# Performance work log

Hardware: AMD Instinct MI355X
Metric: run time of the kernel (lower is better)

The kernel has to match this reference:

```python
import jax, jax.numpy as jnp
import numpy as np

N_HEADS = 8
EMBED_DIM = 512
HEAD_DIM = EMBED_DIM // N_HEADS
INPUT_DIM = 512


def setup_inputs() -> dict:
    key = jax.random.key(0)
    ks = jax.random.split(key, 9)
    B, N = 4, 2048
    s_in = 1.0 / np.sqrt(INPUT_DIM)
    s_e = 1.0 / np.sqrt(EMBED_DIM)
    return {
        "q": jax.random.normal(ks[0], (B, N, INPUT_DIM), dtype=jnp.float32),
        "wq": jax.random.uniform(ks[1], (EMBED_DIM, INPUT_DIM), jnp.float32, -s_in, s_in),
        "bq": jax.random.uniform(ks[2], (EMBED_DIM,), jnp.float32, -s_in, s_in),
        "wk": jax.random.uniform(ks[3], (EMBED_DIM, INPUT_DIM), jnp.float32, -s_in, s_in),
        "bk": jax.random.uniform(ks[4], (EMBED_DIM,), jnp.float32, -s_in, s_in),
        "wv": jax.random.uniform(ks[5], (EMBED_DIM, INPUT_DIM), jnp.float32, -s_in, s_in),
        "bv": jax.random.uniform(ks[6], (EMBED_DIM,), jnp.float32, -s_in, s_in),
        "wo": jax.random.uniform(ks[7], (EMBED_DIM, EMBED_DIM), jnp.float32, -s_e, s_e),
        "bo": jax.random.uniform(ks[8], (EMBED_DIM,), jnp.float32, -s_e, s_e),
    }


def reference(q, wq, bq, wk, bk, wv, bv, wo, bo):
    B, N, _ = q.shape
    # linear projections (torch Linear: x @ W.T + b)
    Q = (q @ wq.T + bq).reshape(B, N, N_HEADS, HEAD_DIM).transpose(0, 2, 1, 3)
    K = (q @ wk.T + bk).reshape(B, N, N_HEADS, HEAD_DIM).transpose(0, 2, 1, 3)
    V = (q @ wv.T + bv).reshape(B, N, N_HEADS, HEAD_DIM).transpose(0, 2, 1, 3)
    scores = jnp.einsum("bhqd,bhkd->bhqk", Q, K) / jnp.sqrt(
        jnp.asarray(HEAD_DIM, dtype=q.dtype)
    )
    weights = jax.nn.softmax(scores, axis=-1)
    out = jnp.einsum("bhqk,bhkd->bhqd", weights, V)  # [B,H,N,Dh]
    out = out.transpose(0, 2, 1, 3).reshape(B, N, EMBED_DIM)
    return out @ wo.T + bo
```

## Files before the change

### kernel.cpp

```cpp
#include <hip/hip_runtime.h>
#include <hip/hip_bf16.h>
#include <math.h>

#define SEQ    2048
#define DH     64
#define EMB    512
#define INDIM  512
#define NHEADS 8
#define BATCH  4
#define MTOT   (BATCH * SEQ)

typedef __attribute__((ext_vector_type(8))) short bf16x8;
typedef __attribute__((ext_vector_type(4))) float f32x4;

__device__ __forceinline__ ushort f2bf(float x) {
  union { float f; unsigned u; } v; v.f = x;
  unsigned r = v.u + 0x7FFFu + ((v.u >> 16) & 1u);
  return (ushort)(r >> 16);
}

__device__ __forceinline__ unsigned cvt_pk_bf16(float lo, float hi) {
  unsigned r;
  asm("v_cvt_pk_bf16_f32 %0, %1, %2" : "=v"(r) : "v"(lo), "v"(hi));
  return r;
}

__device__ __forceinline__ float fast_exp2(float x) {
  float r;
  asm("v_exp_f32 %0, %1" : "=v"(r) : "v"(x));
  return r;
}

__device__ __forceinline__ void permswap32(unsigned &x, unsigned &y) {
  asm("v_permlane32_swap_b32 %0, %1" : "+v"(x), "+v"(y));
}

__global__ __launch_bounds__(256) void conv_bf16(const float* __restrict__ src,
                                                 ushort* __restrict__ dst, int n8) {
  const int i = blockIdx.x * 256 + threadIdx.x;
  if (i >= n8) return;
  const float4 a = ((const float4*)src)[i * 2];
  const float4 b = ((const float4*)src)[i * 2 + 1];
  uint4 o;
  o.x = cvt_pk_bf16(a.x, a.y);
  o.y = cvt_pk_bf16(a.z, a.w);
  o.z = cvt_pk_bf16(b.x, b.y);
  o.w = cvt_pk_bf16(b.z, b.w);
  ((uint4*)dst)[i] = o;
}

__global__ __launch_bounds__(256) void conv_bf16_w4(
    const float* __restrict__ w0, const float* __restrict__ w1,
    const float* __restrict__ w2, const float* __restrict__ w3,
    ushort* __restrict__ dst, int n8per) {
  const int i = blockIdx.x * 256 + threadIdx.x;
  if (i >= n8per) return;
  const float* src = (blockIdx.y == 0) ? w0 : (blockIdx.y == 1) ? w1
                   : (blockIdx.y == 2) ? w2 : w3;
  ushort* d = dst + (size_t)blockIdx.y * n8per * 8;
  const float4 a = ((const float4*)src)[i * 2];
  const float4 b = ((const float4*)src)[i * 2 + 1];
  uint4 o;
  o.x = cvt_pk_bf16(a.x, a.y);
  o.y = cvt_pk_bf16(a.z, a.w);
  o.z = cvt_pk_bf16(b.x, b.y);
  o.w = cvt_pk_bf16(b.z, b.w);
  ((uint4*)d)[i] = o;
}

template <int MODE>
__global__ __launch_bounds__(256) void mfma_gemm(
    const ushort* __restrict__ A, const ushort* __restrict__ W,
    const float* __restrict__ b0, const float* __restrict__ b1,
    const float* __restrict__ b2,
    ushort* __restrict__ outQ, ushort* __restrict__ outK,
    ushort* __restrict__ outVT, float* __restrict__ outF) {
  __shared__ __align__(16) char smem[MODE == 0 ? 35840 : 16384];
  ushort* As = (ushort*)smem;
  ushort* Bs = (ushort*)(smem + 8192);
  ushort* Tl = (ushort*)smem;
  ushort* Tl2 = (ushort*)smem;

  const int bm = blockIdx.x * 128;
  const int bn = blockIdx.y * 128;
  const int tid = threadIdx.x;
  const int wave = tid >> 6, lane = tid & 63;
  const int g = lane >> 4, ln = lane & 15;
  const int wr = wave >> 1, wc = wave & 1;

  f32x4 acc[4][4];
#pragma unroll
  for (int m = 0; m < 4; ++m)
#pragma unroll
    for (int n = 0; n < 4; ++n) acc[m][n] = (f32x4){0.f, 0.f, 0.f, 0.f};

  const size_t a_base = (size_t)(bm + wave * 16 + (lane >> 2)) * INDIM + (lane & 3) * 8;
  const size_t b_base = (size_t)(bn + wave * 16 + (lane >> 2)) * INDIM + (lane & 3) * 8;
  ushort* ldsA0 = As + wave * 512;
  ushort* ldsA1 = As + 2048 + wave * 512;
  ushort* ldsB0 = Bs + wave * 512;
  ushort* ldsB1 = Bs + 2048 + wave * 512;

  for (int k0 = 0; k0 < INDIM; k0 += 32) {
    __syncthreads();
    __builtin_amdgcn_global_load_lds(
        (const __attribute__((address_space(1))) void*)(A + a_base + k0),
        (__attribute__((address_space(3))) void*)ldsA0, 16, 0, 0);
    __builtin_amdgcn_global_load_lds(
        (const __attribute__((address_space(1))) void*)(A + a_base + 64 * INDIM + k0),
        (__attribute__((address_space(3))) void*)ldsA1, 16, 0, 0);
    __builtin_amdgcn_global_load_lds(
        (const __attribute__((address_space(1))) void*)(W + b_base + k0),
        (__attribute__((address_space(3))) void*)ldsB0, 16, 0, 0);
    __builtin_amdgcn_global_load_lds(
        (const __attribute__((address_space(1))) void*)(W + b_base + 64 * INDIM + k0),
        (__attribute__((address_space(3))) void*)ldsB1, 16, 0, 0);
    __syncthreads();

    bf16x8 af[4], bfv[4];
#pragma unroll
    for (int m = 0; m < 4; ++m)
      af[m] = *(const bf16x8*)&As[(64 * wr + 16 * m + ln) * 32 + 8 * g];
#pragma unroll
    for (int n = 0; n < 4; ++n)
      bfv[n] = *(const bf16x8*)&Bs[(64 * wc + 16 * n + ln) * 32 + 8 * g];
#pragma unroll
    for (int m = 0; m < 4; ++m)
#pragma unroll
      for (int n = 0; n < 4; ++n)
        acc[m][n] = __builtin_amdgcn_mfma_f32_16x16x32_bf16(af[m], bfv[n], acc[m][n], 0, 0, 0);
  }

  if (MODE == 1) {
#pragma unroll
    for (int n = 0; n < 4; ++n) {
      const int e = bn + 64 * wc + 16 * n + ln;
      const float bv = b0[e];
#pragma unroll
      for (int m = 0; m < 4; ++m)
#pragma unroll
        for (int r = 0; r < 4; ++r) {
          const int row = bm + 64 * wr + 16 * m + 4 * g + r;
          outF[(size_t)row * EMB + e] = acc[m][n][r] + bv;
        }
    }
    return;
  }

  const int which = bn >> 9;
  const float* bias = (which == 0) ? b0 : (which == 1) ? b1 : b2;

  if (which < 2) {
    const float scl = (which == 0) ? 0.18033688f : 1.0f;
    ushort* dst = (which == 0) ? outQ : outK;
    __syncthreads();
#pragma unroll
    for (int n = 0; n < 4; ++n) {
      const int cl = 64 * wc + 16 * n + ln;
      const float bv = bias[(bn & 511) + cl];
#pragma unroll
      for (int m = 0; m < 4; ++m)
#pragma unroll
        for (int r = 0; r < 4; ++r) {
          const int rl = 64 * wr + 16 * m + 4 * g + r;
          Tl2[rl * 136 + cl] = f2bf((acc[m][n][r] + bv) * scl);
        }
    }
    __syncthreads();
#pragma unroll
    for (int j = 0; j < 8; ++j) {
      const int cid = j * 256 + tid;
      const int seg = cid >> 3;
      const int l8 = cid & 7;
      const int rl = seg >> 1, half = seg & 1;
      const int row = bm + rl;
      const int b = row >> 11, nn = row & (SEQ - 1);
      const int h = ((bn & 511) >> 6) + half;
      const bf16x8 v = *(const bf16x8*)&Tl2[rl * 136 + half * 64 + l8 * 8];
      *(bf16x8*)&dst[(((size_t)(b * NHEADS + h) * SEQ) + nn) * DH + l8 * 8] = v;
    }
  } else {
    __syncthreads();
#pragma unroll
    for (int n = 0; n < 4; ++n) {
      const int cl = 64 * wc + 16 * n + ln;
      const float bv = bias[(bn & 511) + cl];
#pragma unroll
      for (int m = 0; m < 4; ++m)
#pragma unroll
        for (int r = 0; r < 4; ++r) {
          const int rl = 64 * wr + 16 * m + 4 * g + r;
          Tl[cl * 140 + rl] = f2bf(acc[m][n][r] + bv);
        }
    }
    __syncthreads();
    const int c = tid >> 1;
    const int rh = (tid & 1) * 64;
    const int e = (bn & 511) + c;
    const int h = e >> 6, d = e & 63;
    const int b = bm >> 11;
    const int nn0 = (bm & (SEQ - 1)) + rh;
    ushort* drow = outVT + (((size_t)(b * NHEADS + h) * DH) + d) * SEQ + nn0;
#pragma unroll
    for (int j = 0; j < 8; ++j)
      *(bf16x8*)&drow[j * 8] = *(const bf16x8*)&Tl[c * 140 + rh + j * 8];
  }
}

__global__ __launch_bounds__(256) void attn_mfma(const ushort* __restrict__ Q,
                                                 const ushort* __restrict__ K,
                                                 const ushort* __restrict__ VT,
                                                 ushort* __restrict__ O) {
  __shared__ __align__(16) ushort Kl[2][64 * 72];
  __shared__ __align__(16) ushort Vl[2][64 * 72];

  const int tid = threadIdx.x;
  const int wave = tid >> 6, lane = tid & 63;
  const int g = lane >> 4, ln = lane & 15;

  const int orig = blockIdx.x;
  const int swz = (orig & 7) * 64 + (orig >> 3);
  const int bh = swz >> 4;
  const int qx = swz & 15;
  const int qbase = qx * 128 + wave * 32;

  const ushort* Qb = Q + ((size_t)bh * SEQ + qbase) * DH;
  const ushort* Kb = K + (size_t)bh * SEQ * DH;
  const ushort* Vb = VT + (size_t)bh * DH * SEQ;

  const bf16x8 qfA0 = *(const bf16x8*)&Qb[ln * DH + 8 * g];
  const bf16x8 qfA1 = *(const bf16x8*)&Qb[ln * DH + 32 + 8 * g];
  const bf16x8 qfB0 = *(const bf16x8*)&Qb[(16 + ln) * DH + 8 * g];
  const bf16x8 qfB1 = *(const bf16x8*)&Qb[(16 + ln) * DH + 32 + 8 * g];

  bf16x8 vones;
#pragma unroll
  for (int i = 0; i < 8; ++i) vones[i] = (short)0x3F80;

  f32x4 oaccA[4], oaccB[4];
  f32x4 oaccDA = (f32x4){0.f, 0.f, 0.f, 0.f};
  f32x4 oaccDB = (f32x4){0.f, 0.f, 0.f, 0.f};
#pragma unroll
  for (int t = 0; t < 4; ++t) {
    oaccA[t] = (f32x4){0.f, 0.f, 0.f, 0.f};
    oaccB[t] = (f32x4){0.f, 0.f, 0.f, 0.f};
  }

  const int skv = tid >> 3, sd = (tid & 7) * 8;
  const int dt = tid >> 2, kc = (tid & 3) * 8;
  const int pr0 = skv ^ (((((skv >> 2) ^ (skv >> 3)) & 1)) * 12);
  const int s32 = skv + 32;
  const int pr1 = s32 ^ (((((s32 >> 2) ^ (s32 >> 3)) & 1)) * 12);

  bf16x8 k0v = *(const bf16x8*)&Kb[(size_t)skv * DH + sd];
  bf16x8 k1v = *(const bf16x8*)&Kb[(size_t)(32 + skv) * DH + sd];
  bf16x8 v0v = *(const bf16x8*)&Vb[(size_t)dt * SEQ + kc];
  bf16x8 v1v = *(const bf16x8*)&Vb[(size_t)dt * SEQ + 32 + kc];
  *(bf16x8*)&Kl[0][pr0 * 72 + sd] = k0v;
  *(bf16x8*)&Kl[0][pr1 * 72 + sd] = k1v;
  *(bf16x8*)&Vl[0][dt * 72 + kc] = v0v;
  *(bf16x8*)&Vl[0][dt * 72 + 32 + kc] = v1v;
  k0v = *(const bf16x8*)&Kb[(size_t)(64 + skv) * DH + sd];
  k1v = *(const bf16x8*)&Kb[(size_t)(96 + skv) * DH + sd];
  v0v = *(const bf16x8*)&Vb[(size_t)dt * SEQ + 64 + kc];
  v1v = *(const bf16x8*)&Vb[(size_t)dt * SEQ + 96 + kc];
  asm volatile("s_waitcnt lgkmcnt(0)" ::: "memory");
  __builtin_amdgcn_s_barrier();

  for (int it = 0; it < 32; ++it) {
    const int cur = it & 1;
    ushort* Kc = Kl[cur];
    ushort* Vc = Vl[cur];

    if (it < 31) {
      ushort* Kn = Kl[cur ^ 1];
      ushort* Vn = Vl[cur ^ 1];
      *(bf16x8*)&Kn[pr0 * 72 + sd] = k0v;
      *(bf16x8*)&Kn[pr1 * 72 + sd] = k1v;
      *(bf16x8*)&Vn[dt * 72 + kc] = v0v;
      *(bf16x8*)&Vn[dt * 72 + 32 + kc] = v1v;
    }
    {
      const int nxt = (it + 2 < 32) ? (it + 2) * 64 : 31 * 64;
      k0v = *(const bf16x8*)&Kb[(size_t)(nxt + skv) * DH + sd];
      k1v = *(const bf16x8*)&Kb[(size_t)(nxt + 32 + skv) * DH + sd];
      v0v = *(const bf16x8*)&Vb[(size_t)dt * SEQ + nxt + kc];
      v1v = *(const bf16x8*)&Vb[(size_t)dt * SEQ + nxt + 32 + kc];
    }

    bf16x8 ka[4][2], vb[2][4];
#pragma unroll
    for (int t = 0; t < 4; ++t) {
      ka[t][0] = *(const bf16x8*)&Kc[(16 * t + ln) * 72 + 8 * g];
      ka[t][1] = *(const bf16x8*)&Kc[(16 * t + ln) * 72 + 32 + 8 * g];
    }
#pragma unroll
    for (int c = 0; c < 2; ++c)
#pragma unroll
      for (int t = 0; t < 4; ++t)
        vb[c][t] = *(const bf16x8*)&Vc[(16 * t + ln) * 72 + 32 * c + 8 * g];

    f32x4 sA0 = (f32x4){0.f, 0.f, 0.f, 0.f};
    f32x4 sA1 = sA0, sA2 = sA0, sA3 = sA0;
    f32x4 sB0 = sA0, sB1 = sA0, sB2 = sA0, sB3 = sA0;
    __builtin_amdgcn_s_setprio(1);
    sA0 = __builtin_amdgcn_mfma_f32_16x16x32_bf16(ka[0][0], qfA0, sA0, 0, 0, 0);
    sB0 = __builtin_amdgcn_mfma_f32_16x16x32_bf16(ka[0][0], qfB0, sB0, 0, 0, 0);
    sA1 = __builtin_amdgcn_mfma_f32_16x16x32_bf16(ka[1][0], qfA0, sA1, 0, 0, 0);
    sB1 = __builtin_amdgcn_mfma_f32_16x16x32_bf16(ka[1][0], qfB0, sB1, 0, 0, 0);
    sA2 = __builtin_amdgcn_mfma_f32_16x16x32_bf16(ka[2][0], qfA0, sA2, 0, 0, 0);
    sB2 = __builtin_amdgcn_mfma_f32_16x16x32_bf16(ka[2][0], qfB0, sB2, 0, 0, 0);
    sA3 = __builtin_amdgcn_mfma_f32_16x16x32_bf16(ka[3][0], qfA0, sA3, 0, 0, 0);
    sB3 = __builtin_amdgcn_mfma_f32_16x16x32_bf16(ka[3][0], qfB0, sB3, 0, 0, 0);
    sA0 = __builtin_amdgcn_mfma_f32_16x16x32_bf16(ka[0][1], qfA1, sA0, 0, 0, 0);
    sB0 = __builtin_amdgcn_mfma_f32_16x16x32_bf16(ka[0][1], qfB1, sB0, 0, 0, 0);
    sA1 = __builtin_amdgcn_mfma_f32_16x16x32_bf16(ka[1][1], qfA1, sA1, 0, 0, 0);
    sB1 = __builtin_amdgcn_mfma_f32_16x16x32_bf16(ka[1][1], qfB1, sB1, 0, 0, 0);
    sA2 = __builtin_amdgcn_mfma_f32_16x16x32_bf16(ka[2][1], qfA1, sA2, 0, 0, 0);
    sB2 = __builtin_amdgcn_mfma_f32_16x16x32_bf16(ka[2][1], qfB1, sB2, 0, 0, 0);
    sA3 = __builtin_amdgcn_mfma_f32_16x16x32_bf16(ka[3][1], qfA1, sA3, 0, 0, 0);
    sB3 = __builtin_amdgcn_mfma_f32_16x16x32_bf16(ka[3][1], qfB1, sB3, 0, 0, 0);
    __builtin_amdgcn_s_setprio(0);

    float pA0[4], pA1[4], pA2[4], pA3[4];
    float pB0[4], pB1[4], pB2[4], pB3[4];
#pragma unroll
    for (int r = 0; r < 4; ++r) {
      pA0[r] = fast_exp2(sA0[r]);
      pA1[r] = fast_exp2(sA1[r]);
      pA2[r] = fast_exp2(sA2[r]);
      pA3[r] = fast_exp2(sA3[r]);
      pB0[r] = fast_exp2(sB0[r]);
      pB1[r] = fast_exp2(sB1[r]);
      pB2[r] = fast_exp2(sB2[r]);
      pB3[r] = fast_exp2(sB3[r]);
    }

    unsigned aa0 = cvt_pk_bf16(pA0[0], pA0[1]);
    unsigned aa2 = cvt_pk_bf16(pA1[0], pA1[1]);
    unsigned aa1 = cvt_pk_bf16(pA0[2], pA0[3]);
    unsigned aa3 = cvt_pk_bf16(pA1[2], pA1[3]);
    permswap32(aa0, aa2);
    permswap32(aa1, aa3);
    unsigned ab0 = cvt_pk_bf16(pA2[0], pA2[1]);
    unsigned ab2 = cvt_pk_bf16(pA3[0], pA3[1]);
    unsigned ab1 = cvt_pk_bf16(pA2[2], pA2[3]);
    unsigned ab3 = cvt_pk_bf16(pA3[2], pA3[3]);
    permswap32(ab0, ab2);
    permswap32(ab1, ab3);
    unsigned ba0 = cvt_pk_bf16(pB0[0], pB0[1]);
    unsigned ba2 = cvt_pk_bf16(pB1[0], pB1[1]);
    unsigned ba1 = cvt_pk_bf16(pB0[2], pB0[3]);
    unsigned ba3 = cvt_pk_bf16(pB1[2], pB1[3]);
    permswap32(ba0, ba2);
    permswap32(ba1, ba3);
    unsigned bb0 = cvt_pk_bf16(pB2[0], pB2[1]);
    unsigned bb2 = cvt_pk_bf16(pB3[0], pB3[1]);
    unsigned bb1 = cvt_pk_bf16(pB2[2], pB2[3]);
    unsigned bb3 = cvt_pk_bf16(pB3[2], pB3[3]);
    permswap32(bb0, bb2);
    permswap32(bb1, bb3);
    union { unsigned u[4]; bf16x8 v; } paA0, paA1, paB0, paB1;
    paA0.u[0] = aa0; paA0.u[1] = aa1; paA0.u[2] = aa2; paA0.u[3] = aa3;
    paA1.u[0] = ab0; paA1.u[1] = ab1; paA1.u[2] = ab2; paA1.u[3] = ab3;
    paB0.u[0] = ba0; paB0.u[1] = ba1; paB0.u[2] = ba2; paB0.u[3] = ba3;
    paB1.u[0] = bb0; paB1.u[1] = bb1; paB1.u[2] = bb2; paB1.u[3] = bb3;

    __builtin_amdgcn_s_setprio(1);
#pragma unroll
    for (int t = 0; t < 4; ++t) {
      oaccA[t] = __builtin_amdgcn_mfma_f32_16x16x32_bf16(paA0.v, vb[0][t], oaccA[t], 0, 0, 0);
      oaccB[t] = __builtin_amdgcn_mfma_f32_16x16x32_bf16(paB0.v, vb[0][t], oaccB[t], 0, 0, 0);
      oaccA[t] = __builtin_amdgcn_mfma_f32_16x16x32_bf16(paA1.v, vb[1][t], oaccA[t], 0, 0, 0);
      oaccB[t] = __builtin_amdgcn_mfma_f32_16x16x32_bf16(paB1.v, vb[1][t], oaccB[t], 0, 0, 0);
    }
    oaccDA = __builtin_amdgcn_mfma_f32_16x16x32_bf16(paA0.v, vones, oaccDA, 0, 0, 0);
    oaccDB = __builtin_amdgcn_mfma_f32_16x16x32_bf16(paB0.v, vones, oaccDB, 0, 0, 0);
    oaccDA = __builtin_amdgcn_mfma_f32_16x16x32_bf16(paA1.v, vones, oaccDA, 0, 0, 0);
    oaccDB = __builtin_amdgcn_mfma_f32_16x16x32_bf16(paB1.v, vones, oaccDB, 0, 0, 0);
    __builtin_amdgcn_s_setprio(0);

    asm volatile("s_waitcnt lgkmcnt(0)" ::: "memory");
    __builtin_amdgcn_s_barrier();
  }

  const int b = bh >> 3, h = bh & 7;
#pragma unroll
  for (int r = 0; r < 4; ++r) {
    const float irA = 1.0f / oaccDA[r];
    const float irB = 1.0f / oaccDB[r];
    ushort* opA = O + ((size_t)(b * SEQ) + qbase + 4 * g + r) * EMB + h * 64;
    ushort* opB = O + ((size_t)(b * SEQ) + qbase + 16 + 4 * g + r) * EMB + h * 64;
#pragma unroll
    for (int t = 0; t < 4; ++t) {
      opA[16 * t + ln] = f2bf(oaccA[t][r] * irA);
      opB[16 * t + ln] = f2bf(oaccB[t][r] * irB);
    }
  }
}

extern "C" void kernel_launch(void* const* d_in, const int* in_sizes, int n_in,
                              void* d_out, int out_size, void* d_ws, size_t ws_size,
                              hipStream_t stream) {
  const float* q  = (const float*)d_in[0];
  const float* wq = (const float*)d_in[1];
  const float* bq = (const float*)d_in[2];
  const float* wk = (const float*)d_in[3];
  const float* bk = (const float*)d_in[4];
  const float* wv = (const float*)d_in[5];
  const float* bv = (const float*)d_in[6];
  const float* wo = (const float*)d_in[7];
  const float* bo = (const float*)d_in[8];
  float* out = (float*)d_out;

  const size_t XSZ = (size_t)MTOT * INDIM;
  const size_t WSZ = (size_t)EMB * INDIM;
  const size_t QSZ = (size_t)BATCH * NHEADS * SEQ * DH;
  ushort* wsX = (ushort*)d_ws;
  ushort* wsW = wsX + XSZ;
  ushort* wsQ = wsW + 4 * WSZ;
  ushort* wsK = wsQ + QSZ;
  ushort* wsVT = wsK + QSZ;
  ushort* wsA = wsVT + QSZ;

  const dim3 blk(256);

  conv_bf16<<<dim3(XSZ / 8 / 256), blk, 0, stream>>>(q, wsX, XSZ / 8);
  conv_bf16_w4<<<dim3(WSZ / 8 / 256, 4), blk, 0, stream>>>(wq, wk, wv, wo, wsW, WSZ / 8);

  mfma_gemm<0><<<dim3(MTOT / 128, 1536 / 128), blk, 0, stream>>>(
      wsX, wsW, bq, bk, bv, wsQ, wsK, wsVT, nullptr);

  attn_mfma<<<dim3(512), blk, 0, stream>>>(wsQ, wsK, wsVT, wsA);

  mfma_gemm<1><<<dim3(MTOT / 128, EMB / 128), blk, 0, stream>>>(
      wsA, wsW + 3 * WSZ, bo, nullptr, nullptr, nullptr, nullptr, nullptr, out);
}
```

Baseline: 100.9 us.

## Double attention KV tile to 128 and halve output-projection M tile

The attention kernel now stages 128 KV rows per iteration instead of 64, running two 64-row sub-steps per barrier. This halves the number of loop iterations and block-wide barriers and issues larger prefetches. The output-projection GEMM uses a 64-row M tile, doubling its grid from 256 to 512 blocks to fill more CUs. In exchange, attention LDS use and register pressure rise, which may lower occupancy, and the smaller GEMM tile has less data reuse per block.

```diff
diff --git a/kernel.cpp b/kernel.cpp
--- a/kernel.cpp
+++ b/kernel.cpp
@@ -75,22 +75,24 @@
     const float* __restrict__ b2,
     ushort* __restrict__ outQ, ushort* __restrict__ outK,
     ushort* __restrict__ outVT, float* __restrict__ outF) {
-  __shared__ __align__(16) char smem[MODE == 0 ? 35840 : 16384];
+  constexpr int BM = (MODE == 0) ? 128 : 64;
+  constexpr int MF = (MODE == 0) ? 4 : 2;
+  __shared__ __align__(16) char smem[MODE == 0 ? 35840 : 12288];
   ushort* As = (ushort*)smem;
-  ushort* Bs = (ushort*)(smem + 8192);
+  ushort* Bs = (ushort*)(smem + (MODE == 0 ? 8192 : 4096));
   ushort* Tl = (ushort*)smem;
   ushort* Tl2 = (ushort*)smem;
 
-  const int bm = blockIdx.x * 128;
+  const int bm = blockIdx.x * BM;
   const int bn = blockIdx.y * 128;
   const int tid = threadIdx.x;
   const int wave = tid >> 6, lane = tid & 63;
   const int g = lane >> 4, ln = lane & 15;
   const int wr = wave >> 1, wc = wave & 1;
 
-  f32x4 acc[4][4];
-#pragma unroll
-  for (int m = 0; m < 4; ++m)
+  f32x4 acc[MF][4];
+#pragma unroll
+  for (int m = 0; m < MF; ++m)
 #pragma unroll
     for (int n = 0; n < 4; ++n) acc[m][n] = (f32x4){0.f, 0.f, 0.f, 0.f};
 
@@ -106,9 +108,10 @@
     __builtin_amdgcn_global_load_lds(
         (const __attribute__((address_space(1))) void*)(A + a_base + k0),
         (__attribute__((address_space(3))) void*)ldsA0, 16, 0, 0);
-    __builtin_amdgcn_global_load_lds(
-        (const __attribute__((address_space(1))) void*)(A + a_base + 64 * INDIM + k0),
-        (__attribute__((address_space(3))) void*)ldsA1, 16, 0, 0);
+    if (MODE == 0)
+      __builtin_amdgcn_global_load_lds(
+          (const __attribute__((address_space(1))) void*)(A + a_base + 64 * INDIM + k0),
+          (__attribute__((address_space(3))) void*)ldsA1, 16, 0, 0);
     __builtin_amdgcn_global_load_lds(
         (const __attribute__((address_space(1))) void*)(W + b_base + k0),
         (__attribute__((address_space(3))) void*)ldsB0, 16, 0, 0);
@@ -117,15 +120,15 @@
         (__attribute__((address_space(3))) void*)ldsB1, 16, 0, 0);
     __syncthreads();
 
-    bf16x8 af[4], bfv[4];
-#pragma unroll
-    for (int m = 0; m < 4; ++m)
-      af[m] = *(const bf16x8*)&As[(64 * wr + 16 * m + ln) * 32 + 8 * g];
+    bf16x8 af[MF], bfv[4];
+#pragma unroll
+    for (int m = 0; m < MF; ++m)
+      af[m] = *(const bf16x8*)&As[((MODE == 0 ? 64 : 32) * wr + 16 * m + ln) * 32 + 8 * g];
 #pragma unroll
     for (int n = 0; n < 4; ++n)
       bfv[n] = *(const bf16x8*)&Bs[(64 * wc + 16 * n + ln) * 32 + 8 * g];
 #pragma unroll
-    for (int m = 0; m < 4; ++m)
+    for (int m = 0; m < MF; ++m)
 #pragma unroll
       for (int n = 0; n < 4; ++n)
         acc[m][n] = __builtin_amdgcn_mfma_f32_16x16x32_bf16(af[m], bfv[n], acc[m][n], 0, 0, 0);
@@ -137,10 +140,10 @@
       const int e = bn + 64 * wc + 16 * n + ln;
       const float bv = b0[e];
 #pragma unroll
-      for (int m = 0; m < 4; ++m)
+      for (int m = 0; m < MF; ++m)
 #pragma unroll
         for (int r = 0; r < 4; ++r) {
-          const int row = bm + 64 * wr + 16 * m + 4 * g + r;
+          const int row = bm + 32 * wr + 16 * m + 4 * g + r;
           outF[(size_t)row * EMB + e] = acc[m][n][r] + bv;
         }
     }
@@ -211,8 +214,8 @@
                                                  const ushort* __restrict__ K,
                                                  const ushort* __restrict__ VT,
                                                  ushort* __restrict__ O) {
-  __shared__ __align__(16) ushort Kl[2][64 * 72];
-  __shared__ __align__(16) ushort Vl[2][64 * 72];
+  __shared__ __align__(16) ushort Kl[2][128 * 72];
+  __shared__ __align__(16) ushort Vl[2][64 * 136];
 
   const int tid = threadIdx.x;
   const int wave = tid >> 6, lane = tid & 63;
@@ -248,137 +251,149 @@
 
   const int skv = tid >> 3, sd = (tid & 7) * 8;
   const int dt = tid >> 2, kc = (tid & 3) * 8;
-  const int pr0 = skv ^ (((((skv >> 2) ^ (skv >> 3)) & 1)) * 12);
-  const int s32 = skv + 32;
-  const int pr1 = s32 ^ (((((s32 >> 2) ^ (s32 >> 3)) & 1)) * 12);
-
-  bf16x8 k0v = *(const bf16x8*)&Kb[(size_t)skv * DH + sd];
-  bf16x8 k1v = *(const bf16x8*)&Kb[(size_t)(32 + skv) * DH + sd];
-  bf16x8 v0v = *(const bf16x8*)&Vb[(size_t)dt * SEQ + kc];
-  bf16x8 v1v = *(const bf16x8*)&Vb[(size_t)dt * SEQ + 32 + kc];
-  *(bf16x8*)&Kl[0][pr0 * 72 + sd] = k0v;
-  *(bf16x8*)&Kl[0][pr1 * 72 + sd] = k1v;
-  *(bf16x8*)&Vl[0][dt * 72 + kc] = v0v;
-  *(bf16x8*)&Vl[0][dt * 72 + 32 + kc] = v1v;
-  k0v = *(const bf16x8*)&Kb[(size_t)(64 + skv) * DH + sd];
-  k1v = *(const bf16x8*)&Kb[(size_t)(96 + skv) * DH + sd];
-  v0v = *(const bf16x8*)&Vb[(size_t)dt * SEQ + 64 + kc];
-  v1v = *(const bf16x8*)&Vb[(size_t)dt * SEQ + 96 + kc];
+  int pr[4];
+#pragma unroll
+  for (int j = 0; j < 4; ++j) {
+    const int row = skv + 32 * j;
+    pr[j] = row ^ (((((row >> 2) ^ (row >> 3)) & 1)) * 12);
+  }
+
+  bf16x8 kv[4], vv[4];
+#pragma unroll
+  for (int j = 0; j < 4; ++j) {
+    kv[j] = *(const bf16x8*)&Kb[(size_t)(skv + 32 * j) * DH + sd];
+    vv[j] = *(const bf16x8*)&Vb[(size_t)dt * SEQ + kc + 32 * j];
+  }
+#pragma unroll
+  for (int j = 0; j < 4; ++j) {
+    *(bf16x8*)&Kl[0][pr[j] * 72 + sd] = kv[j];
+    *(bf16x8*)&Vl[0][dt * 136 + kc + 32 * j] = vv[j];
+  }
+#pragma unroll
+  for (int j = 0; j < 4; ++j) {
+    kv[j] = *(const bf16x8*)&Kb[(size_t)(128 + skv + 32 * j) * DH + sd];
+    vv[j] = *(const bf16x8*)&Vb[(size_t)dt * SEQ + 128 + kc + 32 * j];
+  }
   asm volatile("s_waitcnt lgkmcnt(0)" ::: "memory");
   __builtin_amdgcn_s_barrier();
 
-  for (int it = 0; it < 32; ++it) {
+  for (int it = 0; it < 16; ++it) {
     const int cur = it & 1;
-    ushort* Kc = Kl[cur];
-    ushort* Vc = Vl[cur];
-
-    if (it < 31) {
+    const ushort* Kc = Kl[cur];
+    const ushort* Vc = Vl[cur];
+
+    if (it < 15) {
       ushort* Kn = Kl[cur ^ 1];
       ushort* Vn = Vl[cur ^ 1];
-      *(bf16x8*)&Kn[pr0 * 72 + sd] = k0v;
-      *(bf16x8*)&Kn[pr1 * 72 + sd] = k1v;
-      *(bf16x8*)&Vn[dt * 72 + kc] = v0v;
-      *(bf16x8*)&Vn[dt * 72 + 32 + kc] = v1v;
+#pragma unroll
+      for (int j = 0; j < 4; ++j) {
+        *(bf16x8*)&Kn[pr[j] * 72 + sd] = kv[j];
+        *(bf16x8*)&Vn[dt * 136 + kc + 32 * j] = vv[j];
+      }
     }
     {
-      const int nxt = (it + 2 < 32) ? (it + 2) * 64 : 31 * 64;
-      k0v = *(const bf16x8*)&Kb[(size_t)(nxt + skv) * DH + sd];
-      k1v = *(const bf16x8*)&Kb[(size_t)(nxt + 32 + skv) * DH + sd];
-      v0v = *(const bf16x8*)&Vb[(size_t)dt * SEQ + nxt + kc];
-      v1v = *(const bf16x8*)&Vb[(size_t)dt * SEQ + nxt + 32 + kc];
-    }
-
-    bf16x8 ka[4][2], vb[2][4];
-#pragma unroll
-    for (int t = 0; t < 4; ++t) {
-      ka[t][0] = *(const bf16x8*)&Kc[(16 * t + ln) * 72 + 8 * g];
-      ka[t][1] = *(const bf16x8*)&Kc[(16 * t + ln) * 72 + 32 + 8 * g];
-    }
-#pragma unroll
-    for (int c = 0; c < 2; ++c)
-#pragma unroll
-      for (int t = 0; t < 4; ++t)
-        vb[c][t] = *(const bf16x8*)&Vc[(16 * t + ln) * 72 + 32 * c + 8 * g];
-
-    f32x4 sA0 = (f32x4){0.f, 0.f, 0.f, 0.f};
-    f32x4 sA1 = sA0, sA2 = sA0, sA3 = sA0;
-    f32x4 sB0 = sA0, sB1 = sA0, sB2 = sA0, sB3 = sA0;
-    __builtin_amdgcn_s_setprio(1);
-    sA0 = __builtin_amdgcn_mfma_f32_16x16x32_bf16(ka[0][0], qfA0, sA0, 0, 0, 0);
-    sB0 = __builtin_amdgcn_mfma_f32_16x16x32_bf16(ka[0][0], qfB0, sB0, 0, 0, 0);
-    sA1 = __builtin_amdgcn_mfma_f32_16x16x32_bf16(ka[1][0], qfA0, sA1, 0, 0, 0);
-    sB1 = __builtin_amdgcn_mfma_f32_16x16x32_bf16(ka[1][0], qfB0, sB1, 0, 0, 0);
-    sA2 = __builtin_amdgcn_mfma_f32_16x16x32_bf16(ka[2][0], qfA0, sA2, 0, 0, 0);
-    sB2 = __builtin_amdgcn_mfma_f32_16x16x32_bf16(ka[2][0], qfB0, sB2, 0, 0, 0);
-    sA3 = __builtin_amdgcn_mfma_f32_16x16x32_bf16(ka[3][0], qfA0, sA3, 0, 0, 0);
-    sB3 = __builtin_amdgcn_mfma_f32_16x16x32_bf16(ka[3][0], qfB0, sB3, 0, 0, 0);
-    sA0 = __builtin_amdgcn_mfma_f32_16x16x32_bf16(ka[0][1], qfA1, sA0, 0, 0, 0);
-    sB0 = __builtin_amdgcn_mfma_f32_16x16x32_bf16(ka[0][1], qfB1, sB0, 0, 0, 0);
-    sA1 = __builtin_amdgcn_mfma_f32_16x16x32_bf16(ka[1][1], qfA1, sA1, 0, 0, 0);
-    sB1 = __builtin_amdgcn_mfma_f32_16x16x32_bf16(ka[1][1], qfB1, sB1, 0, 0, 0);
-    sA2 = __builtin_amdgcn_mfma_f32_16x16x32_bf16(ka[2][1], qfA1, sA2, 0, 0, 0);
-    sB2 = __builtin_amdgcn_mfma_f32_16x16x32_bf16(ka[2][1], qfB1, sB2, 0, 0, 0);
-    sA3 = __builtin_amdgcn_mfma_f32_16x16x32_bf16(ka[3][1], qfA1, sA3, 0, 0, 0);
-    sB3 = __builtin_amdgcn_mfma_f32_16x16x32_bf16(ka[3][1], qfB1, sB3, 0, 0, 0);
-    __builtin_amdgcn_s_setprio(0);
-
-    float pA0[4], pA1[4], pA2[4], pA3[4];
-    float pB0[4], pB1[4], pB2[4], pB3[4];
-#pragma unroll
-    for (int r = 0; r < 4; ++r) {
-      pA0[r] = fast_exp2(sA0[r]);
-      pA1[r] = fast_exp2(sA1[r]);
-      pA2[r] = fast_exp2(sA2[r]);
-      pA3[r] = fast_exp2(sA3[r]);
-      pB0[r] = fast_exp2(sB0[r]);
-      pB1[r] = fast_exp2(sB1[r]);
-      pB2[r] = fast_exp2(sB2[r]);
-      pB3[r] = fast_exp2(sB3[r]);
-    }
-
-    unsigned aa0 = cvt_pk_bf16(pA0[0], pA0[1]);
-    unsigned aa2 = cvt_pk_bf16(pA1[0], pA1[1]);
-    unsigned aa1 = cvt_pk_bf16(pA0[2], pA0[3]);
-    unsigned aa3 = cvt_pk_bf16(pA1[2], pA1[3]);
-    permswap32(aa0, aa2);
-    permswap32(aa1, aa3);
-    unsigned ab0 = cvt_pk_bf16(pA2[0], pA2[1]);
-    unsigned ab2 = cvt_pk_bf16(pA3[0], pA3[1]);
-    unsigned ab1 = cvt_pk_bf16(pA2[2], pA2[3]);
-    unsigned ab3 = cvt_pk_bf16(pA3[2], pA3[3]);
-    permswap32(ab0, ab2);
-    permswap32(ab1, ab3);
-    unsigned ba0 = cvt_pk_bf16(pB0[0], pB0[1]);
-    unsigned ba2 = cvt_pk_bf16(pB1[0], pB1[1]);
-    unsigned ba1 = cvt_pk_bf16(pB0[2], pB0[3]);
-    unsigned ba3 = cvt_pk_bf16(pB1[2], pB1[3]);
-    permswap32(ba0, ba2);
-    permswap32(ba1, ba3);
-    unsigned bb0 = cvt_pk_bf16(pB2[0], pB2[1]);
-    unsigned bb2 = cvt_pk_bf16(pB3[0], pB3[1]);
-    unsigned bb1 = cvt_pk_bf16(pB2[2], pB2[3]);
-    unsigned bb3 = cvt_pk_bf16(pB3[2], pB3[3]);
-    permswap32(bb0, bb2);
-    permswap32(bb1, bb3);
-    union { unsigned u[4]; bf16x8 v; } paA0, paA1, paB0, paB1;
-    paA0.u[0] = aa0; paA0.u[1] = aa1; paA0.u[2] = aa2; paA0.u[3] = aa3;
-    paA1.u[0] = ab0; paA1.u[1] = ab1; paA1.u[2] = ab2; paA1.u[3] = ab3;
-    paB0.u[0] = ba0; paB0.u[1] = ba1; paB0.u[2] = ba2; paB0.u[3] = ba3;
-    paB1.u[0] = bb0; paB1.u[1] = bb1; paB1.u[2] = bb2; paB1.u[3] = bb3;
-
-    __builtin_amdgcn_s_setprio(1);
-#pragma unroll
-    for (int t = 0; t < 4; ++t) {
-      oaccA[t] = __builtin_amdgcn_mfma_f32_16x16x32_bf16(paA0.v, vb[0][t], oaccA[t], 0, 0, 0);
-      oaccB[t] = __builtin_amdgcn_mfma_f32_16x16x32_bf16(paB0.v, vb[0][t], oaccB[t], 0, 0, 0);
-      oaccA[t] = __builtin_amdgcn_mfma_f32_16x16x32_bf16(paA1.v, vb[1][t], oaccA[t], 0, 0, 0);
-      oaccB[t] = __builtin_amdgcn_mfma_f32_16x16x32_bf16(paB1.v, vb[1][t], oaccB[t], 0, 0, 0);
-    }
-    oaccDA = __builtin_amdgcn_mfma_f32_16x16x32_bf16(paA0.v, vones, oaccDA, 0, 0, 0);
-    oaccDB = __builtin_amdgcn_mfma_f32_16x16x32_bf16(paB0.v, vones, oaccDB, 0, 0, 0);
-    oaccDA = __builtin_amdgcn_mfma_f32_16x16x32_bf16(paA1.v, vones, oaccDA, 0, 0, 0);
-    oaccDB = __builtin_amdgcn_mfma_f32_16x16x32_bf16(paB1.v, vones, oaccDB, 0, 0, 0);
-    __builtin_amdgcn_s_setprio(0);
+      const int nxt = (it + 2 < 16) ? (it + 2) * 128 : 15 * 128;
+#pragma unroll
+      for (int j = 0; j < 4; ++j) {
+        kv[j] = *(const bf16x8*)&Kb[(size_t)(nxt + skv + 32 * j) * DH + sd];
+        vv[j] = *(const bf16x8*)&Vb[(size_t)dt * SEQ + nxt + kc + 32 * j];
+      }
+    }
+
+#pragma unroll
+    for (int s = 0; s < 2; ++s) {
+      bf16x8 ka[4][2], vb[2][4];
+#pragma unroll
+      for (int t = 0; t < 4; ++t) {
+        ka[t][0] = *(const bf16x8*)&Kc[(64 * s + 16 * t + ln) * 72 + 8 * g];
+        ka[t][1] = *(const bf16x8*)&Kc[(64 * s + 16 * t + ln) * 72 + 32 + 8 * g];
+      }
+#pragma unroll
+      for (int c = 0; c < 2; ++c)
+#pragma unroll
+        for (int t = 0; t < 4; ++t)
+          vb[c][t] = *(const bf16x8*)&Vc[(16 * t + ln) * 136 + 64 * s + 32 * c + 8 * g];
+
+      f32x4 sA0 = (f32x4){0.f, 0.f, 0.f, 0.f};
+      f32x4 sA1 = sA0, sA2 = sA0, sA3 = sA0;
+      f32x4 sB0 = sA0, sB1 = sA0, sB2 = sA0, sB3 = sA0;
+      __builtin_amdgcn_s_setprio(1);
+      sA0 = __builtin_amdgcn_mfma_f32_16x16x32_bf16(ka[0][0], qfA0, sA0, 0, 0, 0);
+      sB0 = __builtin_amdgcn_mfma_f32_16x16x32_bf16(ka[0][0], qfB0, sB0, 0, 0, 0);
+      sA1 = __builtin_amdgcn_mfma_f32_16x16x32_bf16(ka[1][0], qfA0, sA1, 0, 0, 0);
+      sB1 = __builtin_amdgcn_mfma_f32_16x16x32_bf16(ka[1][0], qfB0, sB1, 0, 0, 0);
+      sA2 = __builtin_amdgcn_mfma_f32_16x16x32_bf16(ka[2][0], qfA0, sA2, 0, 0, 0);
+      sB2 = __builtin_amdgcn_mfma_f32_16x16x32_bf16(ka[2][0], qfB0, sB2, 0, 0, 0);
+      sA3 = __builtin_amdgcn_mfma_f32_16x16x32_bf16(ka[3][0], qfA0, sA3, 0, 0, 0);
+      sB3 = __builtin_amdgcn_mfma_f32_16x16x32_bf16(ka[3][0], qfB0, sB3, 0, 0, 0);
+      sA0 = __builtin_amdgcn_mfma_f32_16x16x32_bf16(ka[0][1], qfA1, sA0, 0, 0, 0);
+      sB0 = __builtin_amdgcn_mfma_f32_16x16x32_bf16(ka[0][1], qfB1, sB0, 0, 0, 0);
+      sA1 = __builtin_amdgcn_mfma_f32_16x16x32_bf16(ka[1][1], qfA1, sA1, 0, 0, 0);
+      sB1 = __builtin_amdgcn_mfma_f32_16x16x32_bf16(ka[1][1], qfB1, sB1, 0, 0, 0);
+      sA2 = __builtin_amdgcn_mfma_f32_16x16x32_bf16(ka[2][1], qfA1, sA2, 0, 0, 0);
+      sB2 = __builtin_amdgcn_mfma_f32_16x16x32_bf16(ka[2][1], qfB1, sB2, 0, 0, 0);
+      sA3 = __builtin_amdgcn_mfma_f32_16x16x32_bf16(ka[3][1], qfA1, sA3, 0, 0, 0);
+      sB3 = __builtin_amdgcn_mfma_f32_16x16x32_bf16(ka[3][1], qfB1, sB3, 0, 0, 0);
+      __builtin_amdgcn_s_setprio(0);
+
+      float pA0[4], pA1[4], pA2[4], pA3[4];
+      float pB0[4], pB1[4], pB2[4], pB3[4];
+#pragma unroll
+      for (int r = 0; r < 4; ++r) {
+        pA0[r] = fast_exp2(sA0[r]);
+        pA1[r] = fast_exp2(sA1[r]);
+        pA2[r] = fast_exp2(sA2[r]);
+        pA3[r] = fast_exp2(sA3[r]);
+        pB0[r] = fast_exp2(sB0[r]);
+        pB1[r] = fast_exp2(sB1[r]);
+        pB2[r] = fast_exp2(sB2[r]);
+        pB3[r] = fast_exp2(sB3[r]);
+      }
+
+      unsigned aa0 = cvt_pk_bf16(pA0[0], pA0[1]);
+      unsigned aa2 = cvt_pk_bf16(pA1[0], pA1[1]);
+      unsigned aa1 = cvt_pk_bf16(pA0[2], pA0[3]);
+      unsigned aa3 = cvt_pk_bf16(pA1[2], pA1[3]);
+      permswap32(aa0, aa2);
+      permswap32(aa1, aa3);
+      unsigned ab0 = cvt_pk_bf16(pA2[0], pA2[1]);
+      unsigned ab2 = cvt_pk_bf16(pA3[0], pA3[1]);
+      unsigned ab1 = cvt_pk_bf16(pA2[2], pA2[3]);
+      unsigned ab3 = cvt_pk_bf16(pA3[2], pA3[3]);
+      permswap32(ab0, ab2);
+      permswap32(ab1, ab3);
+      unsigned ba0 = cvt_pk_bf16(pB0[0], pB0[1]);
+      unsigned ba2 = cvt_pk_bf16(pB1[0], pB1[1]);
+      unsigned ba1 = cvt_pk_bf16(pB0[2], pB0[3]);
+      unsigned ba3 = cvt_pk_bf16(pB1[2], pB1[3]);
+      permswap32(ba0, ba2);
+      permswap32(ba1, ba3);
+      unsigned bb0 = cvt_pk_bf16(pB2[0], pB2[1]);
+      unsigned bb2 = cvt_pk_bf16(pB3[0], pB3[1]);
+      unsigned bb1 = cvt_pk_bf16(pB2[2], pB2[3]);
+      unsigned bb3 = cvt_pk_bf16(pB3[2], pB3[3]);
+      permswap32(bb0, bb2);
+      permswap32(bb1, bb3);
+      union { unsigned u[4]; bf16x8 v; } paA0, paA1, paB0, paB1;
+      paA0.u[0] = aa0; paA0.u[1] = aa1; paA0.u[2] = aa2; paA0.u[3] = aa3;
+      paA1.u[0] = ab0; paA1.u[1] = ab1; paA1.u[2] = ab2; paA1.u[3] = ab3;
+      paB0.u[0] = ba0; paB0.u[1] = ba1; paB0.u[2] = ba2; paB0.u[3] = ba3;
+      paB1.u[0] = bb0; paB1.u[1] = bb1; paB1.u[2] = bb2; paB1.u[3] = bb3;
+
+      __builtin_amdgcn_s_setprio(1);
+#pragma unroll
+      for (int t = 0; t < 4; ++t) {
+        oaccA[t] = __builtin_amdgcn_mfma_f32_16x16x32_bf16(paA0.v, vb[0][t], oaccA[t], 0, 0, 0);
+        oaccB[t] = __builtin_amdgcn_mfma_f32_16x16x32_bf16(paB0.v, vb[0][t], oaccB[t], 0, 0, 0);
+        oaccA[t] = __builtin_amdgcn_mfma_f32_16x16x32_bf16(paA1.v, vb[1][t], oaccA[t], 0, 0, 0);
+        oaccB[t] = __builtin_amdgcn_mfma_f32_16x16x32_bf16(paB1.v, vb[1][t], oaccB[t], 0, 0, 0);
+      }
+      oaccDA = __builtin_amdgcn_mfma_f32_16x16x32_bf16(paA0.v, vones, oaccDA, 0, 0, 0);
+      oaccDB = __builtin_amdgcn_mfma_f32_16x16x32_bf16(paB0.v, vones, oaccDB, 0, 0, 0);
+      oaccDA = __builtin_amdgcn_mfma_f32_16x16x32_bf16(paA1.v, vones, oaccDA, 0, 0, 0);
+      oaccDB = __builtin_amdgcn_mfma_f32_16x16x32_bf16(paB1.v, vones, oaccDB, 0, 0, 0);
+      __builtin_amdgcn_s_setprio(0);
+    }
 
     asm volatile("s_waitcnt lgkmcnt(0)" ::: "memory");
     __builtin_amdgcn_s_barrier();
@@ -433,6 +448,6 @@
 
   attn_mfma<<<dim3(512), blk, 0, stream>>>(wsQ, wsK, wsVT, wsA);
 
-  mfma_gemm<1><<<dim3(MTOT / 128, EMB / 128), blk, 0, stream>>>(
+  mfma_gemm<1><<<dim3(MTOT / 64, EMB / 128), blk, 0, stream>>>(
       wsA, wsW + 3 * WSZ, bo, nullptr, nullptr, nullptr, nullptr, nullptr, out);
 }
```

New measurement: 98.89 us. -2.0%, faster.
